# Kernel optimization log

Measured on AMD Instinct MI355X. Metric: run time of the kernel, lower is better.

Reference implementation:

```python
import jax, jax.numpy as jnp
import numpy as np

# Human3.6M-style 17-joint skeleton: joint 0 is the root (pelvis)
PARENTS = np.array([-1, 0, 1, 2, 0, 4, 5, 0, 7, 8, 9, 8, 11, 12, 8, 14, 15])
NUM_JOINTS = 17
NUM_BONES = 16
# Unit T-pose direction operator per joint (row 0 = root, unused)
T_POSE_OPERATORS = np.array([
    [0., 0., 0.],    # 0 pelvis (root)
    [-1., 0., 0.],   # 1 right hip
    [0., -1., 0.],   # 2 right knee
    [0., -1., 0.],   # 3 right ankle
    [1., 0., 0.],    # 4 left hip
    [0., -1., 0.],   # 5 left knee
    [0., -1., 0.],   # 6 left ankle
    [0., 1., 0.],    # 7 spine
    [0., 1., 0.],    # 8 thorax
    [0., 1., 0.],    # 9 neck
    [0., 1., 0.],    # 10 head
    [1., 0., 0.],    # 11 left shoulder
    [1., 0., 0.],    # 12 left elbow
    [1., 0., 0.],    # 13 left wrist
    [-1., 0., 0.],   # 14 right shoulder
    [-1., 0., 0.],   # 15 right elbow
    [-1., 0., 0.],   # 16 right wrist
], dtype=np.float32)

EPS = 1e-8


def _normalize(v):
    return v / jnp.maximum(jnp.linalg.norm(v, axis=-1, keepdims=True), EPS)


def rot6d_to_matrix(r6):
    """Zhou et al. ortho6d -> rotation matrix. r6: [N, 6] -> [N, 3, 3]."""
    x_raw, y_raw = r6[:, 0:3], r6[:, 3:6]
    x = _normalize(x_raw)
    z = _normalize(jnp.cross(x, y_raw))
    y = jnp.cross(z, x)
    # columns of R are x, y, z
    return jnp.stack([x, y, z], axis=-1)  # [N, 3, 3]


def pose_decoder_forward(rotations_repr, bones_lengths_repr, root_positions):
    BL, J, _ = rotations_repr.shape
    B = bones_lengths_repr.shape[0]
    L = BL // B
    # replicate bone lengths over frames: [B, nb] -> [BL, nb, 1]
    bones_length = jnp.broadcast_to(
        bones_lengths_repr[:, None, :], (B, L, NUM_BONES)
    ).reshape(BL, NUM_BONES, 1)

    # rotation matrices [BL, J, 3, 3]
    R = rot6d_to_matrix(rotations_repr.reshape(-1, 6)).reshape(BL, J, 3, 3)

    # T-pose from bone lengths (17-step tree accumulation)
    ops = jnp.asarray(T_POSE_OPERATORS)
    offsets = ops[1:][None, :, :] * bones_length  # [BL, nb, 3]
    t_pose = [jnp.zeros((BL, 3), dtype=rotations_repr.dtype)]
    for j in range(1, NUM_JOINTS):
        t_pose.append(t_pose[PARENTS[j]] + offsets[:, j - 1])

    # forward kinematics: sequential gather+rotate+accumulate over the tree
    positions_world = [root_positions]
    rotations_world = [R[:, 0]]
    for j in range(1, NUM_JOINTS):
        p = int(PARENTS[j])
        off = t_pose[j] - t_pose[p]  # [BL, 3]
        pos = jnp.einsum('bij,bj->bi', rotations_world[p], off) + positions_world[p]
        positions_world.append(pos)
        rotations_world.append(jnp.einsum('bij,bjk->bik', rotations_world[p], R[:, j]))
    return jnp.stack(positions_world, axis=1)  # [BL, 17, 3]


def setup_inputs() -> dict:
    key = jax.random.key(0)
    k1, k2, k3 = jax.random.split(key, 3)
    BL, B = 131072, 512
    rotations_repr = jax.random.normal(k1, (BL, NUM_JOINTS, 6), dtype=jnp.float32)
    bones_lengths_repr = jax.random.uniform(k2, (B, NUM_BONES), dtype=jnp.float32)
    root_positions = jax.random.normal(k3, (BL, 3), dtype=jnp.float32)
    return {
        'rotations_repr': rotations_repr,
        'bones_lengths_repr': bones_lengths_repr,
        'root_positions': root_positions,
    }


def reference(rotations_repr, bones_lengths_repr, root_positions):
    return pose_decoder_forward(rotations_repr, bones_lengths_repr, root_positions)
```

## Files before the change

kernel.cpp:

```cpp
#include <hip/hip_runtime.h>

#define TPB 256

struct M3 { float a[9]; };
struct V3 { float x, y, z; };

__device__ __forceinline__ void fence_lgkm() {
    asm volatile("s_waitcnt lgkmcnt(0)" ::: "memory");
    __builtin_amdgcn_wave_barrier();
}

__device__ __forceinline__ M3 rot6d2(const float2* v) {
    float x0 = v[0].x, x1 = v[0].y, x2 = v[1].x;
    float y0 = v[1].y, y1 = v[2].x, y2 = v[2].y;
    float inx = rsqrtf(fmaxf(x0*x0 + x1*x1 + x2*x2, 1e-16f));
    x0 *= inx; x1 *= inx; x2 *= inx;
    float z0 = x1*y2 - x2*y1;
    float z1 = x2*y0 - x0*y2;
    float z2 = x0*y1 - x1*y0;
    float inz = rsqrtf(fmaxf(z0*z0 + z1*z1 + z2*z2, 1e-16f));
    z0 *= inz; z1 *= inz; z2 *= inz;
    float w0 = z1*x2 - z2*x1;
    float w1 = z2*x0 - z0*x2;
    float w2 = z0*x1 - z1*x0;
    M3 R;
    R.a[0] = x0; R.a[1] = w0; R.a[2] = z0;
    R.a[3] = x1; R.a[4] = w1; R.a[5] = z1;
    R.a[6] = x2; R.a[7] = w2; R.a[8] = z2;
    return R;
}

__device__ __forceinline__ M3 m3mul(const M3& A, const M3& B) {
    M3 C;
#pragma unroll
    for (int r = 0; r < 3; ++r)
#pragma unroll
        for (int c = 0; c < 3; ++c)
            C.a[3*r + c] = A.a[3*r + 0] * B.a[0 + c]
                         + A.a[3*r + 1] * B.a[3 + c]
                         + A.a[3*r + 2] * B.a[6 + c];
    return C;
}

__device__ __forceinline__ V3 step(const M3& P, V3 pp, int axis, float s) {
    V3 q;
    q.x = pp.x + s * P.a[0 + axis];
    q.y = pp.y + s * P.a[3 + axis];
    q.z = pp.z + s * P.a[6 + axis];
    return q;
}

__device__ __forceinline__ void put(float* so, int j, V3 q) {
    so[3*j + 0] = q.x; so[3*j + 1] = q.y; so[3*j + 2] = q.z;
}

__device__ __forceinline__ void fk_from_regs(const float2 v[12][3], float* so,
                                             const float* len,
                                             float rx, float ry, float rz) {
    V3 q0; q0.x = rx; q0.y = ry; q0.z = rz;
    so[0] = rx; so[1] = ry; so[2] = rz;
    M3 W0 = rot6d2(v[0]);

    M3 W1 = m3mul(W0, rot6d2(v[1]));  V3 q1 = step(W0, q0, 0, -len[0]);  put(so, 1, q1);
    M3 W2 = m3mul(W1, rot6d2(v[2]));  V3 q2 = step(W1, q1, 1, -len[1]);  put(so, 2, q2);
                          V3 q3 = step(W2, q2, 1, -len[2]);  put(so, 3, q3);

    M3 W4 = m3mul(W0, rot6d2(v[3]));  V3 q4 = step(W0, q0, 0,  len[3]);  put(so, 4, q4);
    M3 W5 = m3mul(W4, rot6d2(v[4]));  V3 q5 = step(W4, q4, 1, -len[4]);  put(so, 5, q5);
                          V3 q6 = step(W5, q5, 1, -len[5]);  put(so, 6, q6);

    M3 W7 = m3mul(W0, rot6d2(v[5]));  V3 q7 = step(W0, q0, 1,  len[6]);  put(so, 7, q7);
    M3 W8 = m3mul(W7, rot6d2(v[6]));  V3 q8 = step(W7, q7, 1,  len[7]);  put(so, 8, q8);

    M3 W9 = m3mul(W8, rot6d2(v[7]));  V3 q9 = step(W8, q8, 1,  len[8]);  put(so, 9, q9);
                         V3 q10 = step(W9, q9, 1, len[9]);  put(so, 10, q10);

    M3 W11 = m3mul(W8,  rot6d2(v[8]));  V3 q11 = step(W8,  q8,  0, len[10]); put(so, 11, q11);
    M3 W12 = m3mul(W11, rot6d2(v[9]));  V3 q12 = step(W11, q11, 0, len[11]); put(so, 12, q12);
                           V3 q13 = step(W12, q12, 0, len[12]); put(so, 13, q13);

    M3 W14 = m3mul(W8,  rot6d2(v[10])); V3 q14 = step(W8,  q8,  0, -len[13]); put(so, 14, q14);
    M3 W15 = m3mul(W14, rot6d2(v[11])); V3 q15 = step(W14, q14, 0, -len[14]); put(so, 15, q15);
                           V3 q16 = step(W15, q15, 0, -len[15]); put(so, 16, q16);
}

__device__ __forceinline__ void load_sample(const float* __restrict__ rot,
                                            long long gs, float2 v[12][3]) {
    constexpr int UJ[12] = {0, 1, 2, 4, 5, 7, 8, 9, 11, 12, 14, 15};
    const float2* g2 = (const float2*)(rot + (size_t)gs * 102);
#pragma unroll
    for (int u = 0; u < 12; ++u)
#pragma unroll
        for (int k = 0; k < 3; ++k)
            v[u][k] = g2[UJ[u] * 3 + k];
}

__global__ __launch_bounds__(TPB) void PoseDecoder_kernel(
    const float* __restrict__ rot,
    const float* __restrict__ bones,
    const float* __restrict__ root,
    float* __restrict__ out,
    int BL, int L)
{
    __shared__ __align__(16) float s_out[4 * 64 * 51];
    const int wv = threadIdx.x >> 6;
    const int t  = threadIdx.x & 63;
    const long long blk_base = (long long)blockIdx.x * 256;
    const long long base = blk_base + (long long)wv * 64;
    const long long gs = base + t;
    float* so_wave = s_out + wv * (64 * 51);

    const bool fast = (blk_base + 256 <= BL) &&
                      (blk_base / L == (blk_base + 255) / L);

    if (fast) {
        float2 v[12][3];
        load_sample(rot, gs, v);
        float rx = root[gs*3 + 0], ry = root[gs*3 + 1], rz = root[gs*3 + 2];

        const float* bl = bones + (size_t)(blk_base / L) * 16;
        float len[16];
#pragma unroll
        for (int k = 0; k < 16; ++k) len[k] = bl[k];

        fk_from_regs(v, so_wave + t * 51, len, rx, ry, rz);
        fence_lgkm();

        float4* o4 = (float4*)(out + (size_t)base * 51);
        const float4* l4 = (const float4*)so_wave;
#pragma unroll
        for (int r = 0; r < 12; ++r) o4[r * 64 + t] = l4[r * 64 + t];
        if (t < 48) o4[768 + t] = l4[768 + t];
    } else {
        if (gs < BL) {
            float2 v[12][3];
            load_sample(rot, gs, v);
            float rx = root[gs*3+0], ry = root[gs*3+1], rz = root[gs*3+2];
            const float* bl = bones + (size_t)(gs / L) * 16;
            float len[16];
#pragma unroll
            for (int k = 0; k < 16; ++k) len[k] = bl[k];
            float so[51];
            fk_from_regs(v, so, len, rx, ry, rz);
            for (int m = 0; m < 51; ++m) out[gs * 51 + m] = so[m];
        }
    }
}

extern "C" void kernel_launch(void* const* d_in, const int* in_sizes, int n_in,
                              void* d_out, int out_size, void* d_ws, size_t ws_size,
                              hipStream_t stream) {
    const float* rot   = (const float*)d_in[0];
    const float* bones = (const float*)d_in[1];
    const float* root  = (const float*)d_in[2];
    float* out = (float*)d_out;

    int BL = in_sizes[0] / 102;
    int B  = in_sizes[1] / 16;
    int L  = BL / B;

    int grid = (BL + 255) / 256;
    PoseDecoder_kernel<<<grid, TPB, 0, stream>>>(rot, bones, root, out, BL, L);
}
```

Before: 22.03 us.

## Use single-wave blocks, padded LDS staging, and nontemporal vector stores

Shrinks each block to one 64-thread wave and pads the shared staging buffer to a stride of 52 floats, which is meant to cut LDS bank conflicts on the per-thread writes. The readback now gathers scalars with index div/mod arithmetic before issuing nontemporal float4 global stores, so output data does not pollute the cache. The change also adds a minimum-occupancy hint in launch bounds and quadruples the grid size. The trade-off is extra integer arithmetic and four scalar LDS reads per float4 instead of one vector read.

```diff
diff --git a/kernel.cpp b/kernel.cpp
--- a/kernel.cpp
+++ b/kernel.cpp
@@ -1,6 +1,9 @@
 #include <hip/hip_runtime.h>
 
-#define TPB 256
+#define TPB 64
+#define OSTR 52
+
+typedef float __attribute__((ext_vector_type(4))) f32x4;
 
 struct M3 { float a[9]; };
 struct V3 { float x, y, z; };
@@ -95,42 +98,52 @@
             v[u][k] = g2[UJ[u] * 3 + k];
 }
 
-__global__ __launch_bounds__(TPB) void PoseDecoder_kernel(
+__global__ __launch_bounds__(TPB, 4) void PoseDecoder_kernel(
     const float* __restrict__ rot,
     const float* __restrict__ bones,
     const float* __restrict__ root,
     float* __restrict__ out,
     int BL, int L)
 {
-    __shared__ __align__(16) float s_out[4 * 64 * 51];
-    const int wv = threadIdx.x >> 6;
-    const int t  = threadIdx.x & 63;
-    const long long blk_base = (long long)blockIdx.x * 256;
-    const long long base = blk_base + (long long)wv * 64;
+    __shared__ __align__(16) float s_out[TPB * OSTR];
+    const int t = threadIdx.x;
+    const long long base = (long long)blockIdx.x * TPB;
     const long long gs = base + t;
-    float* so_wave = s_out + wv * (64 * 51);
 
-    const bool fast = (blk_base + 256 <= BL) &&
-                      (blk_base / L == (blk_base + 255) / L);
+    const bool fast = (base + TPB <= BL) &&
+                      (base / L == (base + TPB - 1) / L);
 
     if (fast) {
         float2 v[12][3];
         load_sample(rot, gs, v);
         float rx = root[gs*3 + 0], ry = root[gs*3 + 1], rz = root[gs*3 + 2];
 
-        const float* bl = bones + (size_t)(blk_base / L) * 16;
+        const float* bl = bones + (size_t)(base / L) * 16;
         float len[16];
 #pragma unroll
         for (int k = 0; k < 16; ++k) len[k] = bl[k];
 
-        fk_from_regs(v, so_wave + t * 51, len, rx, ry, rz);
+        fk_from_regs(v, s_out + t * OSTR, len, rx, ry, rz);
         fence_lgkm();
 
-        float4* o4 = (float4*)(out + (size_t)base * 51);
-        const float4* l4 = (const float4*)so_wave;
+        float* o = out + (size_t)base * 51;
 #pragma unroll
-        for (int r = 0; r < 12; ++r) o4[r * 64 + t] = l4[r * 64 + t];
-        if (t < 48) o4[768 + t] = l4[768 + t];
+        for (int r = 0; r < 13; ++r) {
+            int f = r * 64 + t;
+            if (r < 12 || t < 48) {
+                int e0 = f * 4;
+                int s0 = e0 / 51, m0 = e0 - s0 * 51;
+                float a0 = s_out[s0 * OSTR + m0];
+                int e1 = e0 + 1; int s1 = e1 / 51, m1 = e1 - s1 * 51;
+                float a1 = s_out[s1 * OSTR + m1];
+                int e2 = e0 + 2; int s2 = e2 / 51, m2 = e2 - s2 * 51;
+                float a2 = s_out[s2 * OSTR + m2];
+                int e3 = e0 + 3; int s3 = e3 / 51, m3 = e3 - s3 * 51;
+                float a3 = s_out[s3 * OSTR + m3];
+                f32x4 w = {a0, a1, a2, a3};
+                __builtin_nontemporal_store(w, (f32x4*)(o + e0));
+            }
+        }
     } else {
         if (gs < BL) {
             float2 v[12][3];
@@ -159,6 +172,6 @@
     int B  = in_sizes[1] / 16;
     int L  = BL / B;
 
-    int grid = (BL + 255) / 256;
+    int grid = (BL + TPB - 1) / TPB;
     PoseDecoder_kernel<<<grid, TPB, 0, stream>>>(rot, bones, root, out, BL, L);
 }
```

New measurement: 21.43 us. 1.03x faster.
